# Optimization experiments

Hardware: AMD Instinct MI355X
Metric: run time of the kernel (lower is better)

The kernel has to match this reference:

```python
import jax, jax.numpy as jnp
import numpy as np

B, NU, NX, NW, NY, T = 64, 64, 128, 128, 32, 2048


def setup_inputs() -> dict:
    key = jax.random.key(0)
    ks = jax.random.split(key, 14)
    u = jax.random.normal(ks[0], (B, NU, T), dtype=jnp.float32)
    # E initialized at identity in the module; add small perturbation so inverse is nontrivial
    E = jnp.eye(NX, dtype=jnp.float32) + 0.01 * jax.random.normal(ks[1], (NX, NX), dtype=jnp.float32)
    # Recurrent matrices scaled for stability over 2048 steps
    F_w = 0.3 * jax.random.normal(ks[2], (NX, NX), dtype=jnp.float32) / np.sqrt(NX)
    F_b = jnp.zeros((NX,), dtype=jnp.float32)
    B1_w = 0.3 * jax.random.normal(ks[3], (NX, NW), dtype=jnp.float32) / np.sqrt(NW)
    B2_w = 0.3 * jax.random.normal(ks[4], (NX, NU), dtype=jnp.float32) / np.sqrt(NU)
    C2tild = jax.random.normal(ks[5], (NW, NX), dtype=jnp.float32) / np.sqrt(NX)
    Dtild = jax.random.normal(ks[6], (NW, NU), dtype=jnp.float32) / np.sqrt(NU)
    bv = jax.random.uniform(ks[7], (NW,), dtype=jnp.float32) - 0.5
    # IQC multipliers: positive (Neuron method is a per-neuron diagonal)
    lam = 0.5 + jax.random.uniform(ks[8], (NW,), dtype=jnp.float32)
    C1_w = jax.random.normal(ks[9], (NY, NX), dtype=jnp.float32) / np.sqrt(NX)
    D11_w = jax.random.normal(ks[10], (NY, NW), dtype=jnp.float32) / np.sqrt(NW)
    D12_w = jax.random.normal(ks[11], (NY, NU), dtype=jnp.float32) / np.sqrt(NU)
    by = jnp.zeros((NY,), dtype=jnp.float32)
    return {"u": u, "E": E, "F_w": F_w, "F_b": F_b, "B1_w": B1_w, "B2_w": B2_w,
            "C2tild": C2tild, "Dtild": Dtild, "bv": bv, "lam": lam,
            "C1_w": C1_w, "D11_w": D11_w, "D12_w": D12_w, "by": by}


def reference(u, E, F_w, F_b, B1_w, B2_w, C2tild, Dtild, bv, lam, C1_w, D11_w, D12_w, by):
    inputs = jnp.transpose(u, (0, 2, 1))          # (b, T, nu)
    b, seq_len, _ = inputs.shape
    nx = F_w.shape[0]
    Einv = jnp.linalg.inv(E)
    inv_lam = 1.0 / lam
    Cv = inv_lam[:, None] * C2tild                 # diag(1/lam) @ C2tild, (nw, nx)
    Dv = inv_lam[:, None] * Dtild                  # (nw, nu)

    h0 = jnp.zeros((b, nx), dtype=inputs.dtype)

    def step(ht, ut):
        vt = ht @ Cv.T + ut @ Dv.T + bv            # (b, nw)
        wt = jax.nn.relu(vt)
        eh = ht @ F_w.T + F_b + wt @ B1_w.T + ut @ B2_w.T
        ht1 = eh @ Einv.T
        return ht1, ht1

    us = jnp.swapaxes(inputs[:, :-1, :], 0, 1)     # (T-1, b, nu)
    _, states_rest = jax.lax.scan(step, h0, us)    # (T-1, b, nx)
    states = jnp.concatenate([h0[None], states_rest], axis=0)  # (T, b, nx)
    states = jnp.swapaxes(states, 0, 1)            # (b, T, nx)

    W = jax.nn.relu(states @ Cv.T + inputs @ Dv.T + bv)        # (b, T, nw)
    yest = states @ C1_w.T + W @ D11_w.T + inputs @ D12_w.T + by  # (b, T, ny)
    return jnp.transpose(yest, (0, 2, 1))          # (b, ny, T)
```

## Files before the change

### kernel.cpp

```cpp
#include <hip/hip_runtime.h>

#define TD 2048

#define OFF_X0    0
#define OFF_X1    16384
#define OFF_TB    32768
#define OFF_W1T   49152
#define OFF_W2T   81920
#define OFF_WGH   98304
#define OFF_BIAS  114688
#define OFF_C1T   114944
#define OFF_D11T  119040
#define OFF_D12T  123136
#define OFF_BY    125184
#define OFF_HST   125216
#define OFF_GHY   135168

typedef float f32x2 __attribute__((ext_vector_type(2)));

__device__ __forceinline__ float quad_sum(float x) {
  int v = __builtin_bit_cast(int, x);
  v = __builtin_amdgcn_update_dpp(0, v, 0xB1, 0xF, 0xF, true);
  x += __builtin_bit_cast(float, v);
  v = __builtin_bit_cast(int, x);
  v = __builtin_amdgcn_update_dpp(0, v, 0x4E, 0xF, 0xF, true);
  x += __builtin_bit_cast(float, v);
  return x;
}

__device__ __forceinline__ void wg_barrier_lds() {
  asm volatile("s_waitcnt lgkmcnt(0)" ::: "memory");
  __builtin_amdgcn_s_barrier();
  __builtin_amdgcn_sched_barrier(0);
}

__global__ void k_prep(const float* __restrict__ E, const float* __restrict__ C2,
                       const float* __restrict__ Dt, const float* __restrict__ D12,
                       const float* __restrict__ bv, const float* __restrict__ by,
                       const float* __restrict__ C1w, const float* __restrict__ D11w,
                       const float* __restrict__ lam, float* __restrict__ ws)
{
  const int n = 59552;
  for (int e = blockIdx.x * blockDim.x + threadIdx.x; e < n; e += gridDim.x * blockDim.x) {
    int x = e;
    if (x < 16384) { int i = x >> 7, j = x & 127;
      ws[OFF_X0 + x] = (i == j ? 2.f : 0.f) - E[x]; continue; }
    x -= 16384;
    if (x < 16384) { int k = x >> 7, r = x & 127;
      ws[OFF_W1T + k * 256 + r] = C2[r * 128 + k] / lam[r]; continue; }
    x -= 16384;
    if (x < 8192) { int k = x >> 7, j = x & 127;
      ws[OFF_WGH + k * 256 + j] = Dt[j * 64 + k] / lam[j]; continue; }
    x -= 8192;
    if (x < 2048) { int k = x >> 5, r = x & 31;
      ws[OFF_D12T + k * 32 + r] = D12[r * 64 + k]; continue; }
    x -= 2048;
    if (x < 128) { ws[OFF_BIAS + x] = bv[x]; continue; }
    x -= 128;
    if (x < 32) { ws[OFF_BY + x] = by[x]; continue; }
    x -= 32;
    if (x < 4096) { int i = x >> 5, r = x & 31;
      ws[OFF_C1T + i * 32 + r] = C1w[r * 128 + i]; continue; }
    x -= 4096;
    if (x < 4096) { int i = x >> 5, r = x & 31;
      ws[OFF_D11T + i * 32 + r] = D11w[r * 128 + i]; continue; }
    x -= 4096;
    ws[OFF_HST + x] = 0.f;
  }
}

__global__ void k_mm1(const float* __restrict__ E, const float* __restrict__ X,
                      float* __restrict__ Tb)
{
  __shared__ float er[128];
  const int i = blockIdx.x, j = threadIdx.x;
  er[j] = E[i * 128 + j];
  __syncthreads();
  float acc = 0.f;
#pragma unroll 8
  for (int m = 0; m < 128; ++m) acc = fmaf(er[m], X[m * 128 + j], acc);
  Tb[i * 128 + j] = acc;
}

__global__ void k_mm2(const float* __restrict__ X, const float* __restrict__ Tb,
                      float* __restrict__ Xn)
{
  __shared__ float xr[128];
  const int i = blockIdx.x, j = threadIdx.x;
  xr[j] = X[i * 128 + j];
  __syncthreads();
  float acc = 0.f;
#pragma unroll 8
  for (int m = 0; m < 128; ++m) acc = fmaf(xr[m], Tb[m * 128 + j], acc);
  Xn[i * 128 + j] = 2.f * X[i * 128 + j] - acc;
}

__global__ void k_fold(const float* __restrict__ Einv, const float* __restrict__ Fw,
                       const float* __restrict__ B1w, const float* __restrict__ B2w,
                       const float* __restrict__ Fb, float* __restrict__ ws)
{
  __shared__ float ei[128];
  const int i = blockIdx.x, tid = threadIdx.x;
  if (tid < 128) ei[tid] = Einv[i * 128 + tid];
  __syncthreads();
  if (tid < 128) {
    float fh = 0.f, bh1 = 0.f;
#pragma unroll 4
    for (int m = 0; m < 128; ++m) {
      fh  = fmaf(ei[m], Fw[m * 128 + tid], fh);
      bh1 = fmaf(ei[m], B1w[m * 128 + tid], bh1);
    }
    ws[OFF_W1T + tid * 256 + 128 + i] = fh;
    ws[OFF_W2T + tid * 128 + i] = bh1;
  } else if (tid < 192) {
    const int k = tid - 128;
    float bh2 = 0.f;
#pragma unroll 4
    for (int m = 0; m < 128; ++m) bh2 = fmaf(ei[m], B2w[m * 64 + k], bh2);
    ws[OFF_WGH + k * 256 + 128 + i] = bh2;
  } else if (tid == 192) {
    float fb = 0.f;
    for (int m = 0; m < 128; ++m) fb = fmaf(ei[m], Fb[m], fb);
    ws[OFF_BIAS + 128 + i] = fb;
  }
}

__global__ __launch_bounds__(256, 1) void k_pre(
    const float* __restrict__ u, const float* __restrict__ WGH,
    const float* __restrict__ bias, float* __restrict__ GHY, int t_base, int Tc)
{
  const int b = blockIdx.y;
  const int tc0 = blockIdx.x * 32;
  const int tid = threadIdx.x;
  __shared__ __align__(16) float wl[64 * 256];
  for (int c = tid; c < 64 * 256 / 4; c += 256)
    *(float4*)&wl[c * 4] = *(const float4*)&WGH[c * 4];
  __syncthreads();
  float acc[32];
  const float bj = bias[tid];
#pragma unroll
  for (int i = 0; i < 32; ++i) acc[i] = bj;
  const float* ub = u + ((size_t)b * 64) * TD + t_base + tc0;
  for (int k = 0; k < 64; ++k) {
    const float* uk = ub + (size_t)k * TD;
    const float w = wl[k * 256 + tid];
#pragma unroll
    for (int c4 = 0; c4 < 8; ++c4) {
      const float4 uv = *(const float4*)&uk[c4 * 4];
      acc[c4 * 4 + 0] = fmaf(w, uv.x, acc[c4 * 4 + 0]);
      acc[c4 * 4 + 1] = fmaf(w, uv.y, acc[c4 * 4 + 1]);
      acc[c4 * 4 + 2] = fmaf(w, uv.z, acc[c4 * 4 + 2]);
      acc[c4 * 4 + 3] = fmaf(w, uv.w, acc[c4 * 4 + 3]);
    }
  }
  float* gout = GHY + ((size_t)b * Tc + tc0) * 256 + tid;
#pragma unroll
  for (int i = 0; i < 32; ++i) gout[(size_t)i * 256] = acc[i];
}

__global__ __launch_bounds__(256, 1) void k_serial(
    const float* __restrict__ W1t, const float* __restrict__ W2t,
    float* __restrict__ GHY, float* __restrict__ hbT, float* __restrict__ hstate,
    int t_base, int Tc)
{
  const int b = blockIdx.x;
  const int tid = threadIdx.x;
  const int lane = tid & 63;
  const int wave = tid >> 6;
  const int q = lane & 3;
  const int rp = lane >> 2;
  const int r0 = wave * 64 + rp * 4;
  const int r2 = wave * 32 + rp * 2;
  const int hq = q * 36;

  __shared__ __align__(16) float hbufs[2][144];
  __shared__ __align__(16) float wl[144];
  __shared__ __align__(16) float pf[128];

  float w1[4][32], w2[2][32];
#pragma unroll
  for (int kk = 0; kk < 32; ++kk) {
    const float4 wq = *(const float4*)&W1t[(q * 32 + kk) * 256 + r0];
    w1[0][kk] = wq.x; w1[1][kk] = wq.y; w1[2][kk] = wq.z; w1[3][kk] = wq.w;
    const f32x2 w2v = *(const f32x2*)&W2t[(q * 32 + kk) * 128 + r2];
    w2[0][kk] = w2v.x; w2[1][kk] = w2v.y;
  }

  if (tid < 128) {
    const float hv0 = hstate[(size_t)b * 128 + tid];
    hbufs[0][(tid >> 5) * 36 + (tid & 31)] = hv0;
    hbT[((size_t)b * 128 + tid) * Tc] = hv0;
  }

  const size_t ghbase = (size_t)b * Tc * 256;
  float4 ghc = *(const float4*)&GHY[ghbase + r0];
  __syncthreads();

  float* hc = hbufs[0];
  float* hn = hbufs[1];

  for (int t = 0; t < Tc; ++t) {
    const int tn = (t + 1 < Tc) ? (t + 1) : t;
    const float4 ghn = *(const float4*)&GHY[ghbase + (size_t)tn * 256 + r0];

    float hv[32];
#pragma unroll
    for (int c = 0; c < 8; ++c) *(float4*)&hv[c * 4] = *(const float4*)&hc[hq + c * 4];
    float a0 = 0.f, a1 = 0.f, a2 = 0.f, a3 = 0.f;
#pragma unroll
    for (int kk = 0; kk < 32; ++kk) {
      const float h = hv[kk];
      a0 = fmaf(w1[0][kk], h, a0);
      a1 = fmaf(w1[1][kk], h, a1);
      a2 = fmaf(w1[2][kk], h, a2);
      a3 = fmaf(w1[3][kk], h, a3);
    }
    a0 = quad_sum(a0); a1 = quad_sum(a1); a2 = quad_sum(a2); a3 = quad_sum(a3);
    float x0 = a0 + ghc.x, x1 = a1 + ghc.y, x2 = a2 + ghc.z, x3 = a3 + ghc.w;
    if (wave < 2) {
      x0 = fmaxf(x0, 0.f); x1 = fmaxf(x1, 0.f);
      x2 = fmaxf(x2, 0.f); x3 = fmaxf(x3, 0.f);
      if (q == 0) {
        *(float4*)&wl[(r0 >> 5) * 36 + (r0 & 31)] = make_float4(x0, x1, x2, x3);
        *(float4*)&GHY[ghbase + (size_t)t * 256 + r0] = make_float4(x0, x1, x2, x3);
      }
    } else if (q == 0) {
      *(float4*)&pf[r0 - 128] = make_float4(x0, x1, x2, x3);
    }
    wg_barrier_lds();
    if (t_base + t == TD - 1) break;

    float wv[32];
#pragma unroll
    for (int c = 0; c < 8; ++c) *(float4*)&wv[c * 4] = *(const float4*)&wl[hq + c * 4];
    float b0 = 0.f, b1 = 0.f;
#pragma unroll
    for (int kk = 0; kk < 32; ++kk) {
      const float w = wv[kk];
      b0 = fmaf(w2[0][kk], w, b0);
      b1 = fmaf(w2[1][kk], w, b1);
    }
    b0 = quad_sum(b0); b1 = quad_sum(b1);
    if (q == 0) {
      const float hp0 = b0 + pf[r2];
      const float hp1 = b1 + pf[r2 + 1];
      *(f32x2*)&hn[(r2 >> 5) * 36 + (r2 & 31)] = (f32x2){hp0, hp1};
      if (t + 1 < Tc) {
        hbT[((size_t)b * 128 + r2) * Tc + (t + 1)] = hp0;
        hbT[((size_t)b * 128 + r2 + 1) * Tc + (t + 1)] = hp1;
      } else {
        hstate[(size_t)b * 128 + r2] = hp0;
        hstate[(size_t)b * 128 + r2 + 1] = hp1;
      }
    }
    wg_barrier_lds();
    float* tp = hc; hc = hn; hn = tp;
    ghc = ghn;
  }
}

__global__ __launch_bounds__(256, 2) void k_post(
    const float* __restrict__ hbT, const float* __restrict__ GHY,
    const float* __restrict__ C1T, const float* __restrict__ D11T,
    const float* __restrict__ D12T, const float* __restrict__ BY,
    const float* __restrict__ u, float* __restrict__ y, int t_base, int Tc)
{
  const int b = blockIdx.y;
  const int tc0 = blockIdx.x * 32;
  const int tid = threadIdx.x;
  __shared__ __align__(16) float hT[128 * 36];
  __shared__ __align__(16) float wT[128 * 36];
  __shared__ __align__(16) float uT[64 * 36];
  {
    const int i = tid >> 1, half = tid & 1;
    const float* hsrc = hbT + ((size_t)b * 128 + i) * Tc + tc0 + half * 16;
    float* hdst = &hT[i * 36 + half * 16];
#pragma unroll
    for (int c = 0; c < 4; ++c) *(float4*)&hdst[c * 4] = *(const float4*)&hsrc[c * 4];
    const float* wsrc = GHY + ((size_t)b * Tc + tc0 + half * 16) * 256 + i;
    float* wdst = &wT[i * 36 + half * 16];
#pragma unroll
    for (int tt = 0; tt < 16; ++tt) wdst[tt] = wsrc[(size_t)tt * 256];
    if (tid < 128) {
      const float* usrc = u + ((size_t)b * 64 + i) * TD + t_base + tc0 + half * 16;
      float* udst = &uT[i * 36 + half * 16];
#pragma unroll
      for (int c = 0; c < 4; ++c) *(float4*)&udst[c * 4] = *(const float4*)&usrc[c * 4];
    }
  }
  __syncthreads();
  const int jp = tid >> 4;
  const int tq = tid & 15;
  float a00 = 0.f, a01 = 0.f, a10 = 0.f, a11 = 0.f;
#pragma unroll 4
  for (int i = 0; i < 128; ++i) {
    const float2 cv = *(const float2*)&C1T[i * 32 + 2 * jp];
    const float2 hv = *(const float2*)&hT[i * 36 + 2 * tq];
    const float2 dv = *(const float2*)&D11T[i * 32 + 2 * jp];
    const float2 wv = *(const float2*)&wT[i * 36 + 2 * tq];
    a00 = fmaf(cv.x, hv.x, a00); a00 = fmaf(dv.x, wv.x, a00);
    a01 = fmaf(cv.x, hv.y, a01); a01 = fmaf(dv.x, wv.y, a01);
    a10 = fmaf(cv.y, hv.x, a10); a10 = fmaf(dv.y, wv.x, a10);
    a11 = fmaf(cv.y, hv.y, a11); a11 = fmaf(dv.y, wv.y, a11);
  }
#pragma unroll 4
  for (int k = 0; k < 64; ++k) {
    const float2 ev = *(const float2*)&D12T[k * 32 + 2 * jp];
    const float2 uv = *(const float2*)&uT[k * 36 + 2 * tq];
    a00 = fmaf(ev.x, uv.x, a00); a01 = fmaf(ev.x, uv.y, a01);
    a10 = fmaf(ev.y, uv.x, a10); a11 = fmaf(ev.y, uv.y, a11);
  }
  const int j0 = 2 * jp;
  const int tA = t_base + tc0 + 2 * tq;
  const float by0 = BY[j0], by1 = BY[j0 + 1];
  float* yo = y + ((size_t)b * 32 + j0) * TD + tA;
  *(float2*)yo = make_float2(a00 + by0, a01 + by0);
  *(float2*)(yo + TD) = make_float2(a10 + by1, a11 + by1);
}

__global__ void k_sentinel(float* out, float mb) {
  if (threadIdx.x == 0 && blockIdx.x == 0) out[0] = -1.0e6f - mb;
}

extern "C" void kernel_launch(void* const* d_in, const int* in_sizes, int n_in,
                              void* d_out, int out_size, void* d_ws, size_t ws_size,
                              hipStream_t stream)
{
  (void)in_sizes; (void)n_in;
  const float* u    = (const float*)d_in[0];
  const float* E    = (const float*)d_in[1];
  const float* Fw   = (const float*)d_in[2];
  const float* Fb   = (const float*)d_in[3];
  const float* B1w  = (const float*)d_in[4];
  const float* B2w  = (const float*)d_in[5];
  const float* C2   = (const float*)d_in[6];
  const float* Dt   = (const float*)d_in[7];
  const float* bv   = (const float*)d_in[8];
  const float* lam  = (const float*)d_in[9];
  const float* C1w  = (const float*)d_in[10];
  const float* D11w = (const float*)d_in[11];
  const float* D12w = (const float*)d_in[12];
  const float* by   = (const float*)d_in[13];
  float* ws = (float*)d_ws;
  float* y = (float*)d_out;

  const size_t avail = ws_size / 4;
  int Tc = TD;
  while (Tc >= 64) {
    const unsigned long long need = OFF_GHY + 24576ull * (unsigned)Tc;
    if (need <= (unsigned long long)avail) break;
    Tc >>= 1;
  }
  if (Tc < 64) {
    hipMemsetAsync(d_out, 0, (size_t)out_size * 4, stream);
    k_sentinel<<<dim3(1), dim3(64), 0, stream>>>(y, (float)(ws_size >> 20));
    return;
  }
  float* GHY = ws + OFF_GHY;
  float* HBT = GHY + 16384ull * (unsigned)Tc;

  k_prep<<<dim3(64), dim3(256), 0, stream>>>(E, C2, Dt, D12w, bv, by, C1w, D11w, lam, ws);

  float* cur = ws + OFF_X0;
  float* nxt = ws + OFF_X1;
  float* Tb = ws + OFF_TB;
  for (int it = 0; it < 4; ++it) {
    k_mm1<<<dim3(128), dim3(128), 0, stream>>>(E, cur, Tb);
    k_mm2<<<dim3(128), dim3(128), 0, stream>>>(cur, Tb, nxt);
    float* t2 = cur; cur = nxt; nxt = t2;
  }
  k_fold<<<dim3(128), dim3(256), 0, stream>>>(cur, Fw, B1w, B2w, Fb, ws);

  for (int t0 = 0; t0 < TD; t0 += Tc) {
    k_pre<<<dim3(Tc / 32, 64), dim3(256), 0, stream>>>(u, ws + OFF_WGH, ws + OFF_BIAS,
                                                       GHY, t0, Tc);
    k_serial<<<dim3(64), dim3(256), 0, stream>>>(ws + OFF_W1T, ws + OFF_W2T,
                                                 GHY, HBT, ws + OFF_HST, t0, Tc);
    k_post<<<dim3(Tc / 32, 64), dim3(256), 0, stream>>>(HBT, GHY, ws + OFF_C1T,
                                                        ws + OFF_D11T, ws + OFF_D12T,
                                                        ws + OFF_BY, u, y, t0, Tc);
  }
}
```

Before: 1.931 ms.

## Spread serial recurrence across 1024 threads with one output row per quad

The serial scan kernel now launches 1024 threads per batch instead of 256. Each 4-lane quad computes one output row instead of four (first matvec) or two (second matvec), cutting the per-step FMA chain length. Weights are repacked into interleaved pairs so each lane can use packed f32x2 FMAs. The cost is more waves per barrier each step, and half the threads sit idle during the second matvec.

```diff
diff --git a/kernel.cpp b/kernel.cpp
--- a/kernel.cpp
+++ b/kernel.cpp
@@ -5,8 +5,8 @@
 #define OFF_X0    0
 #define OFF_X1    16384
 #define OFF_TB    32768
-#define OFF_W1T   49152
-#define OFF_W2T   81920
+#define OFF_WP1   49152
+#define OFF_WP2   81920
 #define OFF_WGH   98304
 #define OFF_BIAS  114688
 #define OFF_C1T   114944
@@ -14,7 +14,7 @@
 #define OFF_D12T  123136
 #define OFF_BY    125184
 #define OFF_HST   125216
-#define OFF_GHY   135168
+#define OFF_GHY   133408
 
 typedef float f32x2 __attribute__((ext_vector_type(2)));
 
@@ -47,7 +47,7 @@
       ws[OFF_X0 + x] = (i == j ? 2.f : 0.f) - E[x]; continue; }
     x -= 16384;
     if (x < 16384) { int k = x >> 7, r = x & 127;
-      ws[OFF_W1T + k * 256 + r] = C2[r * 128 + k] / lam[r]; continue; }
+      ws[OFF_WP1 + (k >> 1) * 512 + r * 2 + (k & 1)] = C2[r * 128 + k] / lam[r]; continue; }
     x -= 16384;
     if (x < 8192) { int k = x >> 7, j = x & 127;
       ws[OFF_WGH + k * 256 + j] = Dt[j * 64 + k] / lam[j]; continue; }
@@ -110,8 +110,8 @@
       fh  = fmaf(ei[m], Fw[m * 128 + tid], fh);
       bh1 = fmaf(ei[m], B1w[m * 128 + tid], bh1);
     }
-    ws[OFF_W1T + tid * 256 + 128 + i] = fh;
-    ws[OFF_W2T + tid * 128 + i] = bh1;
+    ws[OFF_WP1 + (tid >> 1) * 512 + (128 + i) * 2 + (tid & 1)] = fh;
+    ws[OFF_WP2 + (tid >> 1) * 256 + i * 2 + (tid & 1)] = bh1;
   } else if (tid < 192) {
     const int k = tid - 128;
     float bh2 = 0.f;
@@ -158,104 +158,100 @@
   for (int i = 0; i < 32; ++i) gout[(size_t)i * 256] = acc[i];
 }
 
-__global__ __launch_bounds__(256, 1) void k_serial(
-    const float* __restrict__ W1t, const float* __restrict__ W2t,
+__global__ __launch_bounds__(1024, 4) void k_serial(
+    const float* __restrict__ WP1, const float* __restrict__ WP2,
     float* __restrict__ GHY, float* __restrict__ hbT, float* __restrict__ hstate,
     int t_base, int Tc)
 {
   const int b = blockIdx.x;
   const int tid = threadIdx.x;
-  const int lane = tid & 63;
-  const int wave = tid >> 6;
-  const int q = lane & 3;
-  const int rp = lane >> 2;
-  const int r0 = wave * 64 + rp * 4;
-  const int r2 = wave * 32 + rp * 2;
-  const int hq = q * 36;
-
-  __shared__ __align__(16) float hbufs[2][144];
+  const int q = tid & 3;
+  const int R = tid >> 2;
+  const int r2 = R;
+  const int wq = q * 36;
+
+  __shared__ __align__(16) float hb[2][144];
   __shared__ __align__(16) float wl[144];
   __shared__ __align__(16) float pf[128];
 
-  float w1[4][32], w2[2][32];
-#pragma unroll
-  for (int kk = 0; kk < 32; ++kk) {
-    const float4 wq = *(const float4*)&W1t[(q * 32 + kk) * 256 + r0];
-    w1[0][kk] = wq.x; w1[1][kk] = wq.y; w1[2][kk] = wq.z; w1[3][kk] = wq.w;
-    const f32x2 w2v = *(const f32x2*)&W2t[(q * 32 + kk) * 128 + r2];
-    w2[0][kk] = w2v.x; w2[1][kk] = w2v.y;
-  }
+  f32x2 wp1[16];
+  {
+    const float* base = WP1 + (size_t)(q * 16) * 512 + R * 2;
+#pragma unroll
+    for (int kp = 0; kp < 16; ++kp) {
+      wp1[kp].x = *(const volatile float*)(base + kp * 512);
+      wp1[kp].y = *(const volatile float*)(base + kp * 512 + 1);
+    }
+  }
+  f32x2 wp2[16];
+  if (tid < 512) {
+    const float* base = WP2 + (size_t)(q * 16) * 256 + r2 * 2;
+#pragma unroll
+    for (int kp = 0; kp < 16; ++kp) {
+      wp2[kp].x = *(const volatile float*)(base + kp * 256);
+      wp2[kp].y = *(const volatile float*)(base + kp * 256 + 1);
+    }
+  }
+
+  const bool isv = (R < 128);
 
   if (tid < 128) {
-    const float hv0 = hstate[(size_t)b * 128 + tid];
-    hbufs[0][(tid >> 5) * 36 + (tid & 31)] = hv0;
+    const float hv0 = hstate[b * 128 + tid];
+    hb[0][(tid >> 5) * 36 + (tid & 31)] = hv0;
     hbT[((size_t)b * 128 + tid) * Tc] = hv0;
   }
 
   const size_t ghbase = (size_t)b * Tc * 256;
-  float4 ghc = *(const float4*)&GHY[ghbase + r0];
-  __syncthreads();
-
-  float* hc = hbufs[0];
-  float* hn = hbufs[1];
+  float gcur = GHY[ghbase + R];
+  __syncthreads();
+
+  float* hc = hb[0];
+  float* hn = hb[1];
 
   for (int t = 0; t < Tc; ++t) {
     const int tn = (t + 1 < Tc) ? (t + 1) : t;
-    const float4 ghn = *(const float4*)&GHY[ghbase + (size_t)tn * 256 + r0];
-
-    float hv[32];
-#pragma unroll
-    for (int c = 0; c < 8; ++c) *(float4*)&hv[c * 4] = *(const float4*)&hc[hq + c * 4];
-    float a0 = 0.f, a1 = 0.f, a2 = 0.f, a3 = 0.f;
-#pragma unroll
-    for (int kk = 0; kk < 32; ++kk) {
-      const float h = hv[kk];
-      a0 = fmaf(w1[0][kk], h, a0);
-      a1 = fmaf(w1[1][kk], h, a1);
-      a2 = fmaf(w1[2][kk], h, a2);
-      a3 = fmaf(w1[3][kk], h, a3);
-    }
-    a0 = quad_sum(a0); a1 = quad_sum(a1); a2 = quad_sum(a2); a3 = quad_sum(a3);
-    float x0 = a0 + ghc.x, x1 = a1 + ghc.y, x2 = a2 + ghc.z, x3 = a3 + ghc.w;
-    if (wave < 2) {
-      x0 = fmaxf(x0, 0.f); x1 = fmaxf(x1, 0.f);
-      x2 = fmaxf(x2, 0.f); x3 = fmaxf(x3, 0.f);
+    const float gn = GHY[ghbase + (size_t)tn * 256 + R];
+
+    f32x2 acc = {0.f, 0.f};
+#pragma unroll
+    for (int c = 0; c < 8; ++c) {
+      const float4 hv = *(const float4*)&hc[wq + c * 4];
+      acc = __builtin_elementwise_fma(wp1[2 * c],     (f32x2){hv.x, hv.y}, acc);
+      acc = __builtin_elementwise_fma(wp1[2 * c + 1], (f32x2){hv.z, hv.w}, acc);
+    }
+    float A = quad_sum(acc.x + acc.y);
+    float x = A + gcur;
+    if (isv) {
+      x = fmaxf(x, 0.f);
       if (q == 0) {
-        *(float4*)&wl[(r0 >> 5) * 36 + (r0 & 31)] = make_float4(x0, x1, x2, x3);
-        *(float4*)&GHY[ghbase + (size_t)t * 256 + r0] = make_float4(x0, x1, x2, x3);
+        wl[(R >> 5) * 36 + (R & 31)] = x;
+        GHY[ghbase + (size_t)t * 256 + R] = x;
       }
     } else if (q == 0) {
-      *(float4*)&pf[r0 - 128] = make_float4(x0, x1, x2, x3);
+      pf[R - 128] = x;
     }
     wg_barrier_lds();
     if (t_base + t == TD - 1) break;
 
-    float wv[32];
-#pragma unroll
-    for (int c = 0; c < 8; ++c) *(float4*)&wv[c * 4] = *(const float4*)&wl[hq + c * 4];
-    float b0 = 0.f, b1 = 0.f;
-#pragma unroll
-    for (int kk = 0; kk < 32; ++kk) {
-      const float w = wv[kk];
-      b0 = fmaf(w2[0][kk], w, b0);
-      b1 = fmaf(w2[1][kk], w, b1);
-    }
-    b0 = quad_sum(b0); b1 = quad_sum(b1);
-    if (q == 0) {
-      const float hp0 = b0 + pf[r2];
-      const float hp1 = b1 + pf[r2 + 1];
-      *(f32x2*)&hn[(r2 >> 5) * 36 + (r2 & 31)] = (f32x2){hp0, hp1};
-      if (t + 1 < Tc) {
-        hbT[((size_t)b * 128 + r2) * Tc + (t + 1)] = hp0;
-        hbT[((size_t)b * 128 + r2 + 1) * Tc + (t + 1)] = hp1;
-      } else {
-        hstate[(size_t)b * 128 + r2] = hp0;
-        hstate[(size_t)b * 128 + r2 + 1] = hp1;
+    if (tid < 512) {
+      f32x2 acc2 = {0.f, 0.f};
+#pragma unroll
+      for (int c = 0; c < 8; ++c) {
+        const float4 wv = *(const float4*)&wl[wq + c * 4];
+        acc2 = __builtin_elementwise_fma(wp2[2 * c],     (f32x2){wv.x, wv.y}, acc2);
+        acc2 = __builtin_elementwise_fma(wp2[2 * c + 1], (f32x2){wv.z, wv.w}, acc2);
+      }
+      float A2 = quad_sum(acc2.x + acc2.y);
+      if (q == 0) {
+        const float hp = A2 + pf[r2];
+        hn[(r2 >> 5) * 36 + (r2 & 31)] = hp;
+        if (t + 1 < Tc) hbT[((size_t)b * 128 + r2) * Tc + (t + 1)] = hp;
+        else            hstate[b * 128 + r2] = hp;
       }
     }
     wg_barrier_lds();
     float* tp = hc; hc = hn; hn = tp;
-    ghc = ghn;
+    gcur = gn;
   }
 }
 
@@ -374,8 +370,8 @@
   for (int t0 = 0; t0 < TD; t0 += Tc) {
     k_pre<<<dim3(Tc / 32, 64), dim3(256), 0, stream>>>(u, ws + OFF_WGH, ws + OFF_BIAS,
                                                        GHY, t0, Tc);
-    k_serial<<<dim3(64), dim3(256), 0, stream>>>(ws + OFF_W1T, ws + OFF_W2T,
-                                                 GHY, HBT, ws + OFF_HST, t0, Tc);
+    k_serial<<<dim3(64), dim3(1024), 0, stream>>>(ws + OFF_WP1, ws + OFF_WP2,
+                                                  GHY, HBT, ws + OFF_HST, t0, Tc);
     k_post<<<dim3(Tc / 32, 64), dim3(256), 0, stream>>>(HBT, GHY, ws + OFF_C1T,
                                                         ws + OFF_D11T, ws + OFF_D12T,
                                                         ws + OFF_BY, u, y, t0, Tc);
```

Measured after the change: 1.767 ms. 1.09x faster.

## Double serial-recurrence block to 512 threads, halving per-thread rows

Applied to the files above, without the earlier changes.

The serial scan kernel now runs with 512 threads per batch block instead of 256, so each quad of lanes owns two rows of the fused matrix instead of four and one output state row instead of two. The per-step dependent FMA chain roughly halves, shortening the latency of each timestep on the critical path. In exchange, each workgroup barrier now spans eight waves instead of four, and the GHY workspace offset is shifted.

```diff
diff --git a/kernel.cpp b/kernel.cpp
--- a/kernel.cpp
+++ b/kernel.cpp
@@ -14,7 +14,7 @@
 #define OFF_D12T  123136
 #define OFF_BY    125184
 #define OFF_HST   125216
-#define OFF_GHY   135168
+#define OFF_GHY   133408
 
 typedef float f32x2 __attribute__((ext_vector_type(2)));
 
@@ -158,7 +158,7 @@
   for (int i = 0; i < 32; ++i) gout[(size_t)i * 256] = acc[i];
 }
 
-__global__ __launch_bounds__(256, 1) void k_serial(
+__global__ __launch_bounds__(512, 2) void k_serial(
     const float* __restrict__ W1t, const float* __restrict__ W2t,
     float* __restrict__ GHY, float* __restrict__ hbT, float* __restrict__ hstate,
     int t_base, int Tc)
@@ -168,32 +168,32 @@
   const int lane = tid & 63;
   const int wave = tid >> 6;
   const int q = lane & 3;
-  const int rp = lane >> 2;
-  const int r0 = wave * 64 + rp * 4;
-  const int r2 = wave * 32 + rp * 2;
+  const int G = wave * 16 + (lane >> 2);
+  const int r = 2 * G;
   const int hq = q * 36;
 
   __shared__ __align__(16) float hbufs[2][144];
   __shared__ __align__(16) float wl[144];
   __shared__ __align__(16) float pf[128];
 
-  float w1[4][32], w2[2][32];
+  float wa[32], wb[32], wc[32];
 #pragma unroll
   for (int kk = 0; kk < 32; ++kk) {
-    const float4 wq = *(const float4*)&W1t[(q * 32 + kk) * 256 + r0];
-    w1[0][kk] = wq.x; w1[1][kk] = wq.y; w1[2][kk] = wq.z; w1[3][kk] = wq.w;
-    const f32x2 w2v = *(const f32x2*)&W2t[(q * 32 + kk) * 128 + r2];
-    w2[0][kk] = w2v.x; w2[1][kk] = w2v.y;
-  }
+    const f32x2 wv = *(const f32x2*)&W1t[(q * 32 + kk) * 256 + r];
+    wa[kk] = wv.x; wb[kk] = wv.y;
+    wc[kk] = W2t[(q * 32 + kk) * 128 + G];
+  }
+
+  const bool isv = (G < 64);
 
   if (tid < 128) {
-    const float hv0 = hstate[(size_t)b * 128 + tid];
+    const float hv0 = hstate[b * 128 + tid];
     hbufs[0][(tid >> 5) * 36 + (tid & 31)] = hv0;
     hbT[((size_t)b * 128 + tid) * Tc] = hv0;
   }
 
   const size_t ghbase = (size_t)b * Tc * 256;
-  float4 ghc = *(const float4*)&GHY[ghbase + r0];
+  f32x2 ghc = *(const f32x2*)&GHY[ghbase + r];
   __syncthreads();
 
   float* hc = hbufs[0];
@@ -201,31 +201,27 @@
 
   for (int t = 0; t < Tc; ++t) {
     const int tn = (t + 1 < Tc) ? (t + 1) : t;
-    const float4 ghn = *(const float4*)&GHY[ghbase + (size_t)tn * 256 + r0];
+    const f32x2 ghn = *(const f32x2*)&GHY[ghbase + (size_t)tn * 256 + r];
 
     float hv[32];
 #pragma unroll
     for (int c = 0; c < 8; ++c) *(float4*)&hv[c * 4] = *(const float4*)&hc[hq + c * 4];
-    float a0 = 0.f, a1 = 0.f, a2 = 0.f, a3 = 0.f;
+    float A = 0.f, B = 0.f;
 #pragma unroll
     for (int kk = 0; kk < 32; ++kk) {
-      const float h = hv[kk];
-      a0 = fmaf(w1[0][kk], h, a0);
-      a1 = fmaf(w1[1][kk], h, a1);
-      a2 = fmaf(w1[2][kk], h, a2);
-      a3 = fmaf(w1[3][kk], h, a3);
-    }
-    a0 = quad_sum(a0); a1 = quad_sum(a1); a2 = quad_sum(a2); a3 = quad_sum(a3);
-    float x0 = a0 + ghc.x, x1 = a1 + ghc.y, x2 = a2 + ghc.z, x3 = a3 + ghc.w;
-    if (wave < 2) {
+      A = fmaf(wa[kk], hv[kk], A);
+      B = fmaf(wb[kk], hv[kk], B);
+    }
+    A = quad_sum(A); B = quad_sum(B);
+    float x0 = A + ghc.x, x1 = B + ghc.y;
+    if (isv) {
       x0 = fmaxf(x0, 0.f); x1 = fmaxf(x1, 0.f);
-      x2 = fmaxf(x2, 0.f); x3 = fmaxf(x3, 0.f);
       if (q == 0) {
-        *(float4*)&wl[(r0 >> 5) * 36 + (r0 & 31)] = make_float4(x0, x1, x2, x3);
-        *(float4*)&GHY[ghbase + (size_t)t * 256 + r0] = make_float4(x0, x1, x2, x3);
+        *(f32x2*)&wl[(r >> 5) * 36 + (r & 31)] = (f32x2){x0, x1};
+        *(f32x2*)&GHY[ghbase + (size_t)t * 256 + r] = (f32x2){x0, x1};
       }
     } else if (q == 0) {
-      *(float4*)&pf[r0 - 128] = make_float4(x0, x1, x2, x3);
+      *(f32x2*)&pf[r - 128] = (f32x2){x0, x1};
     }
     wg_barrier_lds();
     if (t_base + t == TD - 1) break;
@@ -233,25 +229,15 @@
     float wv[32];
 #pragma unroll
     for (int c = 0; c < 8; ++c) *(float4*)&wv[c * 4] = *(const float4*)&wl[hq + c * 4];
-    float b0 = 0.f, b1 = 0.f;
-#pragma unroll
-    for (int kk = 0; kk < 32; ++kk) {
-      const float w = wv[kk];
-      b0 = fmaf(w2[0][kk], w, b0);
-      b1 = fmaf(w2[1][kk], w, b1);
-    }
-    b0 = quad_sum(b0); b1 = quad_sum(b1);
+    float C = 0.f;
+#pragma unroll
+    for (int kk = 0; kk < 32; ++kk) C = fmaf(wc[kk], wv[kk], C);
+    C = quad_sum(C);
     if (q == 0) {
-      const float hp0 = b0 + pf[r2];
-      const float hp1 = b1 + pf[r2 + 1];
-      *(f32x2*)&hn[(r2 >> 5) * 36 + (r2 & 31)] = (f32x2){hp0, hp1};
-      if (t + 1 < Tc) {
-        hbT[((size_t)b * 128 + r2) * Tc + (t + 1)] = hp0;
-        hbT[((size_t)b * 128 + r2 + 1) * Tc + (t + 1)] = hp1;
-      } else {
-        hstate[(size_t)b * 128 + r2] = hp0;
-        hstate[(size_t)b * 128 + r2 + 1] = hp1;
-      }
+      const float hp = C + pf[G];
+      hn[(G >> 5) * 36 + (G & 31)] = hp;
+      if (t + 1 < Tc) hbT[((size_t)b * 128 + G) * Tc + (t + 1)] = hp;
+      else            hstate[b * 128 + G] = hp;
     }
     wg_barrier_lds();
     float* tp = hc; hc = hn; hn = tp;
@@ -374,7 +360,7 @@
   for (int t0 = 0; t0 < TD; t0 += Tc) {
     k_pre<<<dim3(Tc / 32, 64), dim3(256), 0, stream>>>(u, ws + OFF_WGH, ws + OFF_BIAS,
                                                        GHY, t0, Tc);
-    k_serial<<<dim3(64), dim3(256), 0, stream>>>(ws + OFF_W1T, ws + OFF_W2T,
+    k_serial<<<dim3(64), dim3(512), 0, stream>>>(ws + OFF_W1T, ws + OFF_W2T,
                                                  GHY, HBT, ws + OFF_HST, t0, Tc);
     k_post<<<dim3(Tc / 32, 64), dim3(256), 0, stream>>>(HBT, GHY, ws + OFF_C1T,
                                                         ws + OFF_D11T, ws + OFF_D12T,
```

Result: faster. 1.777 ms (-7.9%).
